# Performance work log

Measured on AMD Instinct MI355X. Metric: run time of the kernel, lower is better.

## Reference

```python
import jax, jax.numpy as jnp
import numpy as np

N, T, D, W, H = 2, 1024, 256, 128, 8
HD = D // H


def setup_inputs() -> dict:
    key = jax.random.key(0)
    ks = jax.random.split(key, 5)
    s = 0.05
    return {
        "inputs": jax.random.normal(ks[0], (N, T, D), jnp.float32),
        "in_proj_w": jax.random.normal(ks[1], (3 * D, D), jnp.float32) * s,
        "in_proj_b": jax.random.normal(ks[2], (3 * D,), jnp.float32) * s,
        "out_w": jax.random.normal(ks[3], (D, D), jnp.float32) * s,
        "out_b": jax.random.normal(ks[4], (D,), jnp.float32) * s,
    }


def reference(inputs, in_proj_w, in_proj_b, out_w, out_b):
    n, t, d = inputs.shape
    # Window with stride=1, lpad='steady': pad W-1 zeros on the left, T_out = T_in
    x = jnp.pad(inputs, ((0, 0), (W - 1, 0), (0, 0)))
    idx = jnp.arange(t)[:, None] + jnp.arange(W)[None, :]  # [T, W]
    windows = x[:, idx]                                    # [N, T, W, D]
    w = windows.reshape(n * t, W, d)
    q = w[:, -1]                                           # [NT, D] (last window element)
    # Faithful to torch: windows.transpose(1,2).reshape(-1, W, D) on contiguous data
    kv = jnp.swapaxes(w, 1, 2).reshape(n * t, W, d)        # [NT, W, D]
    Wq, Wk, Wv = in_proj_w[:d], in_proj_w[d:2 * d], in_proj_w[2 * d:]
    bq, bk, bv = in_proj_b[:d], in_proj_b[d:2 * d], in_proj_b[2 * d:]
    qh = (q @ Wq.T + bq).reshape(n * t, H, HD)             # [NT, H, HD]
    kh = (kv @ Wk.T + bk).reshape(n * t, W, H, HD)
    vh = (kv @ Wv.T + bv).reshape(n * t, W, H, HD)
    scores = jnp.einsum('nhd,nwhd->nhw', qh, kh) / np.float32(np.sqrt(HD))
    # causal warmup mask: disallow key slot j when j < W-1-t (the zero-padded positions)
    tvec = jnp.arange(t)
    mask = jnp.arange(W)[None, :] < (W - 1 - tvec)[:, None]  # [T, W], True = masked
    mask = jnp.broadcast_to(mask[None], (n, t, W)).reshape(n * t, 1, W)
    scores = jnp.where(mask, -jnp.inf, scores)
    attn = jax.nn.softmax(scores, axis=-1)
    out = jnp.einsum('nhw,nwhd->nhd', attn, vh).reshape(n * t, d)
    out = out @ out_w.T + out_b
    return out.reshape(n, t, 1, d)
```

## Files before the change

kernel.cpp:

```cpp
#include <hip/hip_runtime.h>
#include <math.h>

#define NTOK 2048
#define TT   1024
constexpr float SCL = 0.17677669529663687f;

#define OFF_WQT 0
#define OFF_WKT 65536
#define OFF_WVT 131072
#define OFF_OWT 196608
#define OFF_RQ  262144
#define OFF_SB  4456448
#define OFF_CTX 4472832

#define GLOAD_LDS16(g, l)                                                      \
    __builtin_amdgcn_global_load_lds(                                          \
        (const __attribute__((address_space(1))) unsigned int*)(g),            \
        (__attribute__((address_space(3))) unsigned int*)(l), 16, 0, 0)

__global__ __launch_bounds__(256) void k0_transpose(const float* __restrict__ ipw,
                                                    const float* __restrict__ ow,
                                                    float* __restrict__ ws) {
    __shared__ float tile[32][33];
    int bx = blockIdx.x;
    int mat = bx >> 6, tl = bx & 63;
    int tr0 = (tl >> 3) << 5, tc0 = (tl & 7) << 5;
    const float* src;
    float* dst;
    if (mat == 3) { src = ow;             dst = ws + OFF_OWT; }
    else          { src = ipw + mat*65536; dst = ws + OFF_WQT + mat*65536; }
    int c = threadIdx.x & 31, r0 = threadIdx.x >> 5;
    #pragma unroll
    for (int k = 0; k < 4; k++) {
        int r = r0 + k*8;
        tile[r][c] = src[(tr0 + r)*256 + tc0 + c];
    }
    __syncthreads();
    #pragma unroll
    for (int k = 0; k < 4; k++) {
        int r = r0 + k*8;
        dst[(tc0 + r)*256 + tr0 + c] = tile[c][r];
    }
}

__global__ __launch_bounds__(512) void k1_qrq(const float* __restrict__ x,
                                              const float* __restrict__ ipw,
                                              const float* __restrict__ ipb,
                                              float* __restrict__ ws) {
    __shared__ float x8[2048];
    __shared__ float qpart[4096];
    __shared__ float qh[2048];
    extern __shared__ float rqt[];
    const float* wqT = ws + OFF_WQT;
    const float* wk  = ipw + 65536;
    float* rqw = ws + OFF_RQ;
    float* sbw = ws + OFF_SB;
    int tid = threadIdx.x;
    long i0 = (long)blockIdx.x * 8;

    ((float4*)x8)[tid] = ((const float4*)(x + i0*256))[tid];
    __syncthreads();

    int c = tid & 255, half = tid >> 8;
    {
        float qa[8];
        #pragma unroll
        for (int ii = 0; ii < 8; ii++) qa[ii] = 0.f;
        int cc0 = half*128;
        #pragma unroll 8
        for (int cc = cc0; cc < cc0 + 128; cc++) {
            float w = wqT[cc*256 + c];
            #pragma unroll
            for (int ii = 0; ii < 8; ii++) qa[ii] += x8[ii*256 + cc]*w;
        }
        #pragma unroll
        for (int ii = 0; ii < 8; ii++) qpart[(half*8 + ii)*256 + c] = qa[ii];
    }
    __syncthreads();
    if (tid < 256) {
        float b = ipb[tid];
        #pragma unroll
        for (int ii = 0; ii < 8; ii++)
            qh[ii*256 + tid] = qpart[ii*256 + tid] + qpart[(8 + ii)*256 + tid] + b;
    }
    __syncthreads();
    {
        int k = tid & 255, hh = tid >> 8;
        int s = k & 127, par = k >> 7;
        for (int h = hh*4; h < hh*4 + 4; h++) {
            float ra[8];
            #pragma unroll
            for (int ii = 0; ii < 8; ii++) ra[ii] = 0.f;
            #pragma unroll 8
            for (int hd = 0; hd < 32; hd++) {
                float w = wk[(h*32 + hd)*256 + k];
                #pragma unroll
                for (int ii = 0; ii < 8; ii++) ra[ii] += qh[ii*256 + h*32 + hd]*w;
            }
            int h2p = h*2 + par;
            #pragma unroll
            for (int ii = 0; ii < 8; ii++)
                rqt[ii*2112 + h2p*132 + s] = ra[ii]*SCL;
        }
    }
    __syncthreads();
    {
        float4* dst = (float4*)(rqw + i0*2048);
        #pragma unroll
        for (int it = 0; it < 8; it++) {
            int f = it*512 + tid;
            int s = (f & 511) >> 2, q = f & 3;
            int base = it*2112 + s;
            float4 v;
            v.x = rqt[base + (4*q + 0)*132];
            v.y = rqt[base + (4*q + 1)*132];
            v.z = rqt[base + (4*q + 2)*132];
            v.w = rqt[base + (4*q + 3)*132];
            dst[f] = v;
        }
    }
    if (tid < 64) {
        int ii = tid >> 3, h = tid & 7;
        float s = 0.f;
        #pragma unroll 8
        for (int hd = 0; hd < 32; hd++) s += qh[ii*256 + h*32 + hd]*ipb[256 + h*32 + hd];
        sbw[(i0 + ii)*8 + h] = s*SCL;
    }
}

__global__ __launch_bounds__(512) void k2_attn(const float* __restrict__ x,
                                               float* __restrict__ ws) {
    extern __shared__ float sm[];
    float* xw   = sm;
    float* rq2  = sm + 33024;
    float* scp  = sm + 33024 + 2048;
    float* attn = rq2;
    const float* rqw = ws + OFF_RQ;
    const float* sbw = ws + OFF_SB;
    float* ctxw = ws + OFF_CTX;
    int tid = threadIdx.x;
    int i = blockIdx.x;
    int t = i & (TT - 1);
    int w = tid >> 6, lane = tid & 63;

    {
        #pragma unroll
        for (int it = 0; it < 16; it++) {
            int r = it*8 + w;
            int ts = t - 127 + r;
            float* lrow = xw + r*258;
            if (ts >= 0) {
                const float* g = x + (long)(i - 127 + r)*256 + lane*4;
                GLOAD_LDS16(g, lrow);
            } else {
                float4 z = {0.f, 0.f, 0.f, 0.f};
                *(float4*)(lrow + lane*4) = z;
            }
        }
        const float* g = rqw + (long)i*2048 + w*256 + lane*4;
        GLOAD_LDS16(g, rq2 + w*256);
    }
    __syncthreads();

    {
        int jj = tid & 127, q = tid >> 7;
        float a[8];
        #pragma unroll
        for (int h = 0; h < 8; h++) a[h] = 0.f;
        const float4* rq4 = (const float4*)rq2;
        #pragma unroll 4
        for (int s = q*32; s < q*32 + 32; s++) {
            float2 x2 = *(const float2*)&xw[s*258 + 2*jj];
            float4 r0 = rq4[s*4 + 0];
            float4 r1 = rq4[s*4 + 1];
            float4 r2 = rq4[s*4 + 2];
            float4 r3 = rq4[s*4 + 3];
            a[0] += r0.x*x2.x + r0.y*x2.y;
            a[1] += r0.z*x2.x + r0.w*x2.y;
            a[2] += r1.x*x2.x + r1.y*x2.y;
            a[3] += r1.z*x2.x + r1.w*x2.y;
            a[4] += r2.x*x2.x + r2.y*x2.y;
            a[5] += r2.z*x2.x + r2.w*x2.y;
            a[6] += r3.x*x2.x + r3.y*x2.y;
            a[7] += r3.z*x2.x + r3.w*x2.y;
        }
        #pragma unroll
        for (int h = 0; h < 8; h++) scp[h*512 + q*128 + jj] = a[h];
    }
    __syncthreads();

    {
        int h = tid >> 6, l = tid & 63;
        float sb = sbw[i*8 + h];
        float s1 = sb, s2 = sb;
        #pragma unroll
        for (int q = 0; q < 4; q++) {
            s1 += scp[h*512 + q*128 + l];
            s2 += scp[h*512 + q*128 + l + 64];
        }
        int lim = 127 - t;
        bool m1 = l < lim, m2 = (l + 64) < lim;
        if (m1) s1 = -1e30f;
        if (m2) s2 = -1e30f;
        float m = fmaxf(s1, s2);
        #pragma unroll
        for (int d = 1; d < 64; d <<= 1) m = fmaxf(m, __shfl_xor(m, d, 64));
        float e1 = m1 ? 0.f : __expf(s1 - m);
        float e2 = m2 ? 0.f : __expf(s2 - m);
        float sum = e1 + e2;
        #pragma unroll
        for (int d = 1; d < 64; d <<= 1) sum += __shfl_xor(sum, d, 64);
        float r = 1.0f / sum;
        attn[l*8 + h] = e1*r;
        attn[(l + 64)*8 + h] = e2*r;
    }
    __syncthreads();

    {
        int sC = tid & 127, jq = tid >> 7;
        float cac[16];
        #pragma unroll
        for (int c = 0; c < 16; c++) cac[c] = 0.f;
        #pragma unroll 4
        for (int j = jq*32; j < jq*32 + 32; j++) {
            float2 x2 = *(const float2*)&xw[sC*258 + 2*j];
            float4 a0 = *(const float4*)&attn[j*8];
            float4 a1 = *(const float4*)&attn[j*8 + 4];
            cac[0]  += a0.x*x2.x; cac[1]  += a0.y*x2.x; cac[2]  += a0.z*x2.x; cac[3]  += a0.w*x2.x;
            cac[4]  += a1.x*x2.x; cac[5]  += a1.y*x2.x; cac[6]  += a1.z*x2.x; cac[7]  += a1.w*x2.x;
            cac[8]  += a0.x*x2.y; cac[9]  += a0.y*x2.y; cac[10] += a0.z*x2.y; cac[11] += a0.w*x2.y;
            cac[12] += a1.x*x2.y; cac[13] += a1.y*x2.y; cac[14] += a1.z*x2.y; cac[15] += a1.w*x2.y;
        }
        __syncthreads();
        #pragma unroll
        for (int c = 0; c < 16; c++) xw[c*512 + tid] = cac[c];
    }
    __syncthreads();

    if (tid < 256) {
        int k = tid, p = k >> 7;
        float v[8];
        #pragma unroll
        for (int h = 0; h < 8; h++) v[h] = 0.f;
        #pragma unroll
        for (int jq = 0; jq < 4; jq++) {
            int thr = jq*128 + (k & 127);
            #pragma unroll
            for (int h = 0; h < 8; h++) v[h] += xw[(p*8 + h)*512 + thr];
        }
        float4* dst = (float4*)(ctxw + (long)i*2048 + k*8);
        float4 o0 = {v[0], v[1], v[2], v[3]};
        float4 o1 = {v[4], v[5], v[6], v[7]};
        dst[0] = o0; dst[1] = o1;
    }
}

__global__ __launch_bounds__(512) void k3_proj(const float* __restrict__ ipb,
                                               const float* __restrict__ ob,
                                               float* __restrict__ ws,
                                               float* __restrict__ out) {
    extern __shared__ float sm[];
    float* ctx8   = sm;
    float* oppart = sm + 16384;
    float* op     = sm + 16384 + 4096;
    const float* wvT  = ws + OFF_WVT;
    const float* owT  = ws + OFF_OWT;
    const float* ctxw = ws + OFF_CTX;
    int tid = threadIdx.x;
    long i0 = (long)blockIdx.x * 8;

    {
        const float4* src = (const float4*)(ctxw + i0*2048);
        float4* dst = (float4*)ctx8;
        #pragma unroll
        for (int it = 0; it < 8; it++) dst[it*512 + tid] = src[it*512 + tid];
    }
    __syncthreads();

    int c = tid & 255, kh = tid >> 8;
    {
        int h = c >> 5;
        float acc[8];
        #pragma unroll
        for (int ii = 0; ii < 8; ii++) acc[ii] = 0.f;
        #pragma unroll 8
        for (int k = kh*128; k < kh*128 + 128; k++) {
            float w = wvT[k*256 + c];
            #pragma unroll
            for (int ii = 0; ii < 8; ii++) acc[ii] += w*ctx8[ii*2048 + k*8 + h];
        }
        #pragma unroll
        for (int ii = 0; ii < 8; ii++) oppart[(kh*8 + ii)*256 + c] = acc[ii];
    }
    __syncthreads();
    if (tid < 256) {
        float b = ipb[512 + tid];
        #pragma unroll
        for (int ii = 0; ii < 8; ii++)
            op[ii*256 + tid] = oppart[ii*256 + tid] + oppart[(8 + ii)*256 + tid] + b;
    }
    __syncthreads();
    {
        float acc[8];
        #pragma unroll
        for (int ii = 0; ii < 8; ii++) acc[ii] = 0.f;
        #pragma unroll 8
        for (int cc = kh*128; cc < kh*128 + 128; cc++) {
            float w = owT[cc*256 + c];
            #pragma unroll
            for (int ii = 0; ii < 8; ii++) acc[ii] += w*op[ii*256 + cc];
        }
        #pragma unroll
        for (int ii = 0; ii < 8; ii++) oppart[(kh*8 + ii)*256 + c] = acc[ii];
    }
    __syncthreads();
    if (tid < 256) {
        float b = ob[tid];
        #pragma unroll
        for (int ii = 0; ii < 8; ii++)
            out[(i0 + ii)*256 + tid] = oppart[ii*256 + tid] + oppart[(8 + ii)*256 + tid] + b;
    }
}

extern "C" void kernel_launch(void* const* d_in, const int* in_sizes, int n_in,
                              void* d_out, int out_size, void* d_ws, size_t ws_size,
                              hipStream_t stream) {
    const float* x   = (const float*)d_in[0];
    const float* ipw = (const float*)d_in[1];
    const float* ipb = (const float*)d_in[2];
    const float* ow  = (const float*)d_in[3];
    const float* ob  = (const float*)d_in[4];
    float* out = (float*)d_out;
    float* ws  = (float*)d_ws;

    (void)in_sizes; (void)n_in; (void)out_size; (void)ws_size;

    hipFuncSetAttribute(reinterpret_cast<const void*>(k1_qrq),
                        hipFuncAttributeMaxDynamicSharedMemorySize, 67584);
    hipFuncSetAttribute(reinterpret_cast<const void*>(k2_attn),
                        hipFuncAttributeMaxDynamicSharedMemorySize, 156672);
    hipFuncSetAttribute(reinterpret_cast<const void*>(k3_proj),
                        hipFuncAttributeMaxDynamicSharedMemorySize, 90112);

    hipLaunchKernelGGL(k0_transpose, dim3(256),  dim3(256), 0,      stream, ipw, ow, ws);
    hipLaunchKernelGGL(k1_qrq,       dim3(256),  dim3(512), 67584,  stream, x, ipw, ipb, ws);
    hipLaunchKernelGGL(k2_attn,      dim3(2048), dim3(512), 156672, stream, x, ws);
    hipLaunchKernelGGL(k3_proj,      dim3(256),  dim3(512), 90112,  stream, ipb, ob, ws, out);
}
```

Baseline: 184.6 us.

## Repad LDS rows, regroup score loop by head halves, transpose ctx in proj

In the attention kernel, the LDS row stride for the window tile changes from 258 to 260 floats so each lane can read a float4. The score loop is regrouped so each wave handles 4 heads over 4 columns, and the partial-score layout changes to match. In the projection kernel, the per-block context is stored transposed with padding in LDS, so the inner loop reads two float4s instead of eight strided scalars. The cost is more LDS per block and a scattered scalar-store transpose, and the new padding may alter bank-conflict behaviour in the later context loop.

```diff
diff --git a/kernel.cpp b/kernel.cpp
--- a/kernel.cpp
+++ b/kernel.cpp
@@ -132,8 +132,8 @@
                                                float* __restrict__ ws) {
     extern __shared__ float sm[];
     float* xw   = sm;
-    float* rq2  = sm + 33024;
-    float* scp  = sm + 33024 + 2048;
+    float* rq2  = sm + 33280;
+    float* scp  = sm + 33280 + 2048;
     float* attn = rq2;
     const float* rqw = ws + OFF_RQ;
     const float* sbw = ws + OFF_SB;
@@ -148,7 +148,7 @@
         for (int it = 0; it < 16; it++) {
             int r = it*8 + w;
             int ts = t - 127 + r;
-            float* lrow = xw + r*258;
+            float* lrow = xw + r*260;
             if (ts >= 0) {
                 const float* g = x + (long)(i - 127 + r)*256 + lane*4;
                 GLOAD_LDS16(g, lrow);
@@ -163,40 +163,38 @@
     __syncthreads();
 
     {
-        int jj = tid & 127, q = tid >> 7;
-        float a[8];
-        #pragma unroll
-        for (int h = 0; h < 8; h++) a[h] = 0.f;
+        int jj2 = lane;
+        int q = w >> 1, hh = w & 1;
+        float a00=0.f,a01=0.f,a10=0.f,a11=0.f,a20=0.f,a21=0.f,a30=0.f,a31=0.f;
         const float4* rq4 = (const float4*)rq2;
+        int s0 = q*32;
         #pragma unroll 4
-        for (int s = q*32; s < q*32 + 32; s++) {
-            float2 x2 = *(const float2*)&xw[s*258 + 2*jj];
-            float4 r0 = rq4[s*4 + 0];
-            float4 r1 = rq4[s*4 + 1];
-            float4 r2 = rq4[s*4 + 2];
-            float4 r3 = rq4[s*4 + 3];
-            a[0] += r0.x*x2.x + r0.y*x2.y;
-            a[1] += r0.z*x2.x + r0.w*x2.y;
-            a[2] += r1.x*x2.x + r1.y*x2.y;
-            a[3] += r1.z*x2.x + r1.w*x2.y;
-            a[4] += r2.x*x2.x + r2.y*x2.y;
-            a[5] += r2.z*x2.x + r2.w*x2.y;
-            a[6] += r3.x*x2.x + r3.y*x2.y;
-            a[7] += r3.z*x2.x + r3.w*x2.y;
-        }
-        #pragma unroll
-        for (int h = 0; h < 8; h++) scp[h*512 + q*128 + jj] = a[h];
-    }
-    __syncthreads();
-
-    {
-        int h = tid >> 6, l = tid & 63;
+        for (int s = s0; s < s0 + 32; s++) {
+            float4 xv = *(const float4*)&xw[s*260 + 4*jj2];
+            float4 r0 = rq4[s*4 + hh*2];
+            float4 r1 = rq4[s*4 + hh*2 + 1];
+            a00 += r0.x*xv.x + r0.y*xv.y;  a01 += r0.x*xv.z + r0.y*xv.w;
+            a10 += r0.z*xv.x + r0.w*xv.y;  a11 += r0.z*xv.z + r0.w*xv.w;
+            a20 += r1.x*xv.x + r1.y*xv.y;  a21 += r1.x*xv.z + r1.y*xv.w;
+            a30 += r1.z*xv.x + r1.w*xv.y;  a31 += r1.z*xv.z + r1.w*xv.w;
+        }
+        int hb = hh*4;
+        float2* sc2 = (float2*)scp;
+        float2 v0 = {a00, a01}; sc2[q*512 + (hb+0)*64 + jj2] = v0;
+        float2 v1 = {a10, a11}; sc2[q*512 + (hb+1)*64 + jj2] = v1;
+        float2 v2 = {a20, a21}; sc2[q*512 + (hb+2)*64 + jj2] = v2;
+        float2 v3 = {a30, a31}; sc2[q*512 + (hb+3)*64 + jj2] = v3;
+    }
+    __syncthreads();
+
+    {
+        int h = w, l = lane;
         float sb = sbw[i*8 + h];
         float s1 = sb, s2 = sb;
         #pragma unroll
         for (int q = 0; q < 4; q++) {
-            s1 += scp[h*512 + q*128 + l];
-            s2 += scp[h*512 + q*128 + l + 64];
+            s1 += scp[q*1024 + h*128 + l];
+            s2 += scp[q*1024 + h*128 + l + 64];
         }
         int lim = 127 - t;
         bool m1 = l < lim, m2 = (l + 64) < lim;
@@ -223,7 +221,7 @@
         for (int c = 0; c < 16; c++) cac[c] = 0.f;
         #pragma unroll 4
         for (int j = jq*32; j < jq*32 + 32; j++) {
-            float2 x2 = *(const float2*)&xw[sC*258 + 2*j];
+            float2 x2 = *(const float2*)&xw[sC*260 + 2*j];
             float4 a0 = *(const float4*)&attn[j*8];
             float4 a1 = *(const float4*)&attn[j*8 + 4];
             cac[0]  += a0.x*x2.x; cac[1]  += a0.y*x2.x; cac[2]  += a0.z*x2.x; cac[3]  += a0.w*x2.x;
@@ -260,9 +258,9 @@
                                                float* __restrict__ ws,
                                                float* __restrict__ out) {
     extern __shared__ float sm[];
-    float* ctx8   = sm;
-    float* oppart = sm + 16384;
-    float* op     = sm + 16384 + 4096;
+    float* ctx8T  = sm;
+    float* oppart = sm + 18432;
+    float* op     = sm + 18432 + 4096;
     const float* wvT  = ws + OFF_WVT;
     const float* owT  = ws + OFF_OWT;
     const float* ctxw = ws + OFF_CTX;
@@ -271,9 +269,16 @@
 
     {
         const float4* src = (const float4*)(ctxw + i0*2048);
-        float4* dst = (float4*)ctx8;
-        #pragma unroll
-        for (int it = 0; it < 8; it++) dst[it*512 + tid] = src[it*512 + tid];
+        #pragma unroll
+        for (int it = 0; it < 8; it++) {
+            float4 v = src[it*512 + tid];
+            int base = tid*4;
+            #pragma unroll
+            for (int m = 0; m < 4; m++) {
+                int kh8 = base + m;
+                ctx8T[kh8*8 + (kh8 >> 2)*4 + it] = (&v.x)[m];
+            }
+        }
     }
     __syncthreads();
 
@@ -286,8 +291,12 @@
         #pragma unroll 8
         for (int k = kh*128; k < kh*128 + 128; k++) {
             float w = wvT[k*256 + c];
-            #pragma unroll
-            for (int ii = 0; ii < 8; ii++) acc[ii] += w*ctx8[ii*2048 + k*8 + h];
+            int kh8 = k*8 + h;
+            int base = kh8*8 + (kh8 >> 2)*4;
+            float4 c0 = *(const float4*)&ctx8T[base];
+            float4 c1 = *(const float4*)&ctx8T[base + 4];
+            acc[0] += w*c0.x; acc[1] += w*c0.y; acc[2] += w*c0.z; acc[3] += w*c0.w;
+            acc[4] += w*c1.x; acc[5] += w*c1.y; acc[6] += w*c1.z; acc[7] += w*c1.w;
         }
         #pragma unroll
         for (int ii = 0; ii < 8; ii++) oppart[(kh*8 + ii)*256 + c] = acc[ii];
@@ -338,12 +347,12 @@
     hipFuncSetAttribute(reinterpret_cast<const void*>(k1_qrq),
                         hipFuncAttributeMaxDynamicSharedMemorySize, 67584);
     hipFuncSetAttribute(reinterpret_cast<const void*>(k2_attn),
-                        hipFuncAttributeMaxDynamicSharedMemorySize, 156672);
+                        hipFuncAttributeMaxDynamicSharedMemorySize, 157696);
     hipFuncSetAttribute(reinterpret_cast<const void*>(k3_proj),
-                        hipFuncAttributeMaxDynamicSharedMemorySize, 90112);
+                        hipFuncAttributeMaxDynamicSharedMemorySize, 98304);
 
     hipLaunchKernelGGL(k0_transpose, dim3(256),  dim3(256), 0,      stream, ipw, ow, ws);
     hipLaunchKernelGGL(k1_qrq,       dim3(256),  dim3(512), 67584,  stream, x, ipw, ipb, ws);
-    hipLaunchKernelGGL(k2_attn,      dim3(2048), dim3(512), 156672, stream, x, ws);
-    hipLaunchKernelGGL(k3_proj,      dim3(256),  dim3(512), 90112,  stream, ipb, ob, ws, out);
-}
+    hipLaunchKernelGGL(k2_attn,      dim3(2048), dim3(512), 157696, stream, x, ws);
+    hipLaunchKernelGGL(k3_proj,      dim3(256),  dim3(512), 98304,  stream, ipb, ob, ws, out);
+}
```

Result: no change. 185.2 us (+0.3%).
